# Optimization experiments

Hardware: AMD Instinct MI355X
Metric: run time of the kernel (lower is better)

Reference implementation:

```python
import math
import jax
import jax.numpy as jnp
from jax import lax
import numpy as np

LARGE_NUMBER = 1e10
NEG = -1e30  # finite stand-in for -inf (safe for logaddexp grads)
K = 64
TRAIN_ENSEMBLE = 2


def _init_esp(M, k, dtype):
    # log elementary symmetric polys of the empty set: e_0 = 1, e_r>0 = 0
    return jnp.full((M, k + 1), NEG, dtype).at[:, 0].set(0.0)


def _esp_step(carry, th_col):
    # carry: [M, k+1] log e_r; add one item with logit th_col: e_r <- e_r + w*e_{r-1}
    M = carry.shape[0]
    shifted = jnp.concatenate([jnp.full((M, 1), NEG, carry.dtype), carry[:, :-1]], axis=1)
    new = jnp.logaddexp(carry, shifted + th_col[:, None])
    return new, new


def log_ek_sum(theta, k):
    # sum over rows of log e_k(exp(theta_row)); grad wrt theta = exact-k inclusion marginals
    init = _init_esp(theta.shape[0], k, theta.dtype)
    final, _ = lax.scan(lambda c, t: (_esp_step(c, t)[0], None), init, theta.T)
    return final[:, k].sum()


def marginals_exact_k(theta, k):
    return jax.grad(lambda th: log_ek_sum(th, k))(theta)  # [M, N]


def suffix_esp_table(theta, k):
    # T[j] = log elem. symmetric polys of suffix items j..N-1; shape [N+1, M, k+1]
    init = _init_esp(theta.shape[0], k, theta.dtype)
    _, Ts = lax.scan(_esp_step, init, jnp.flip(theta.T, 0))
    return jnp.flip(jnp.concatenate([init[None], Ts], 0), 0)


def sample_exact_k(theta, k, u):
    # sequential conditional sampling of an exact-k subset (conditional Poisson)
    # theta: [M, N], u: [T, M, N] uniforms -> binary samples [T, M, N]
    M, N = theta.shape
    T = u.shape[0]
    Tab = suffix_esp_table(theta, k)  # [N+1, M, k+1]
    ar = jnp.arange(M)

    def step(r, xs):
        th_col, Tc, Tn, u_col = xs  # [M], [M,k+1], [M,k+1], [T,M]
        num = Tn[ar[None, :], jnp.maximum(r - 1, 0)]  # [T, M]
        den = Tc[ar[None, :], r]
        p = jnp.where(r > 0, jnp.exp(th_col[None, :] + num - den), 0.0)
        inc = (u_col < p)
        return r - inc.astype(r.dtype), inc.astype(theta.dtype)

    r0 = jnp.full((T, M), k, jnp.int32)
    _, incs = lax.scan(step, r0, (theta.T, Tab[:-1], Tab[1:], jnp.moveaxis(u, 2, 0)))
    return jnp.moveaxis(incs, 0, 2)  # [T, M, N]


def setup_inputs():
    key = jax.random.key(0)
    k1, k2 = jax.random.split(key)
    scores = jax.random.normal(k1, (64, 4096, 2), jnp.float32)
    u = jax.random.uniform(k2, (TRAIN_ENSEMBLE, 64 * 2, 4096), jnp.float32)
    return {"scores": scores, "u": u}


def reference(scores, u):
    B, Nmax, E = scores.shape
    times_sampled = TRAIN_ENSEMBLE
    local_k = min(K, Nmax)
    flat = scores.transpose(0, 2, 1).reshape(B * E, Nmax)
    N = 2 ** math.ceil(math.log2(Nmax))
    flat = jnp.pad(flat, ((0, 0), (0, N - Nmax)), constant_values=-LARGE_NUMBER)
    marg = marginals_exact_k(flat, local_k)           # [M, N]
    samples = sample_exact_k(flat, local_k, u)        # [T, M, N]
    # straight-through estimator
    samples = lax.stop_gradient(samples - marg[None]) + marg[None]
    samples = samples[..., :Nmax]
    marg = marg[:, :Nmax]
    new_mask = samples.reshape(times_sampled, B, E, Nmax).transpose(0, 1, 3, 2)
    new_marginals = marg.reshape(B, E, Nmax).transpose(0, 2, 1)
    return new_mask, new_marginals
```

## Files before the change

### kernel.cpp

```cpp
#include <hip/hip_runtime.h>
#include <hip/hip_bf16.h>

#define NROWS 128
#define NCOLS 4096
#define KVAL  64
#define NEGV  (-1e30f)
#define LOG2E 1.4426950408889634f
#define LN2   0.6931471805599453f

__device__ float g_suf[(size_t)NROWS * (NCOLS + 1) * 64];
__device__ float g_pre[(size_t)NROWS * (NCOLS + 1) * 64];
__device__ unsigned long long g_mask[(size_t)2 * NROWS * NCOLS];
__device__ unsigned char g_map  [(size_t)2 * NROWS * 64 * 64];
__device__ unsigned char g_entry[(size_t)2 * NROWS * 64];

__device__ __forceinline__ float shr1z(float x) {
    int r = __builtin_amdgcn_update_dpp(0, __float_as_int(x), 0x138, 0xF, 0xF, true);
    return __int_as_float(r);
}
__device__ __forceinline__ float readlane_f(float v, int lane) {
    return __int_as_float(__builtin_amdgcn_readlane(__float_as_int(v), lane));
}
__device__ __forceinline__ float lae_fast(float a, float b) {
    float mx = fmaxf(a, b);
    float d  = fabsf(a - b);
    float e  = __builtin_amdgcn_exp2f(d * -LOG2E);
    return fmaf(__builtin_amdgcn_logf(1.0f + e), LN2, mx);
}

__device__ __forceinline__ float dpp_sum64(float x) {
#define SSTEP(ctrl, rmask) { int t_ = __builtin_amdgcn_update_dpp(0, \
        __float_as_int(x), ctrl, rmask, 0xF, false); x = x + __int_as_float(t_); }
    SSTEP(0x111, 0xF) SSTEP(0x112, 0xF) SSTEP(0x114, 0xF) SSTEP(0x118, 0xF)
    SSTEP(0x142, 0xA) SSTEP(0x143, 0xC)
#undef SSTEP
    return readlane_f(x, 63);
}

__global__ __launch_bounds__(64) void dp_kernel(const float* __restrict__ scores) {
    int blk = blockIdx.x;
    int l = threadIdx.x;
    bool suf = (blk < NROWS);
    int m = suf ? blk : (blk - NROWS);
    float* __restrict__ tab = (suf ? g_suf : g_pre) + (size_t)m * (NCOLS + 1) * 64;
    const float* __restrict__ srow = scores + (size_t)(m >> 1) * (NCOLS * 2) + (m & 1);

    tab[(size_t)(suf ? NCOLS : 0) * 64 + l] = NEGV;
    float s = NEGV;
    if (suf) {
        float tile = srow[(size_t)(NCOLS - 64 + l) * 2];
        for (int t0 = NCOLS - 64; t0 >= 0; t0 -= 64) {
            float nxt = (t0 >= 64) ? srow[(size_t)(t0 - 64 + l) * 2] : 0.0f;
            #pragma unroll
            for (int ss = 63; ss >= 0; --ss) {
                float tht = readlane_f(tile, ss);
                float b = shr1z(s) + tht;
                s = lae_fast(s, b);
                tab[(size_t)(t0 + ss) * 64 + l] = s;
            }
            tile = nxt;
        }
    } else {
        float tile = srow[(size_t)l * 2];
        for (int t0 = 0; t0 < NCOLS; t0 += 64) {
            float nxt = (t0 + 64 < NCOLS) ? srow[(size_t)(t0 + 64 + l) * 2] : 0.0f;
            #pragma unroll
            for (int ss = 0; ss < 64; ++ss) {
                float tht = readlane_f(tile, ss);
                float b = shr1z(s) + tht;
                s = lae_fast(s, b);
                tab[(size_t)(t0 + ss + 1) * 64 + l] = s;
            }
            tile = nxt;
        }
    }
}

__global__ __launch_bounds__(256) void maskA_kernel(const float* __restrict__ scores,
                                                    const float* __restrict__ u) {
    int l = threadIdx.x & 63;
    int wid = threadIdx.x >> 6;
    int unit = blockIdx.x * 4 + wid;
    int m  = unit >> 6;
    int b  = unit & 63;
    int t0 = b << 6;
    const float* __restrict__ S = g_suf + (size_t)m * (NCOLS + 1) * 64;
    const float* __restrict__ srow = scores + (size_t)(m >> 1) * (NCOLS * 2) + (m & 1);
    const float* __restrict__ u0 = u + (size_t)m * NCOLS;
    const float* __restrict__ u1 = u + (size_t)(NROWS + m) * NCOLS;

    float R[65];
    #pragma unroll
    for (int j = 0; j <= 64; ++j) R[j] = S[(size_t)(t0 + j) * 64 + l];

    unsigned long long acc0 = 0, acc1 = 0;
    #pragma unroll
    for (int ss = 0; ss < 64; ++ss) {
        int t = t0 + ss;
        float num = shr1z(R[ss + 1]);
        float den = R[ss];
        float tht = srow[(size_t)t * 2];
        float p = __builtin_amdgcn_exp2f(((num + tht) - den) * LOG2E);
        unsigned long long b0 = __ballot(u0[t] < p);
        unsigned long long b1 = __ballot(u1[t] < p);
        acc0 = (l == ss) ? b0 : acc0;
        acc1 = (l == ss) ? b1 : acc1;
    }
    g_mask[(size_t)m * NCOLS + t0 + l] = acc0;
    g_mask[(size_t)(NROWS + m) * NCOLS + t0 + l] = acc1;

    unsigned int a0lo = (unsigned int)acc0, a0hi = (unsigned int)(acc0 >> 32);
    unsigned int a1lo = (unsigned int)acc1, a1hi = (unsigned int)(acc1 >> 32);
    int r0 = l + 1, r1 = l + 1;
    #pragma unroll
    for (int ss = 0; ss < 64; ++ss) {
        unsigned int m0lo = (unsigned int)__builtin_amdgcn_readlane((int)a0lo, ss);
        unsigned int m0hi = (unsigned int)__builtin_amdgcn_readlane((int)a0hi, ss);
        unsigned int m1lo = (unsigned int)__builtin_amdgcn_readlane((int)a1lo, ss);
        unsigned int m1hi = (unsigned int)__builtin_amdgcn_readlane((int)a1hi, ss);
        unsigned long long msk0 = ((unsigned long long)m0hi << 32) | m0lo;
        unsigned long long msk1 = ((unsigned long long)m1hi << 32) | m1lo;
        int inc0 = (r0 > 0) ? (int)((msk0 >> (r0 - 1)) & 1ULL) : 0;
        int inc1 = (r1 > 0) ? (int)((msk1 >> (r1 - 1)) & 1ULL) : 0;
        r0 -= inc0;
        r1 -= inc1;
    }
    g_map[((size_t)m * 64 + b) * 64 + l] = (unsigned char)r0;
    g_map[((size_t)(NROWS + m) * 64 + b) * 64 + l] = (unsigned char)r1;
}

__global__ __launch_bounds__(256) void scanB_kernel() {
    int c = threadIdx.x;
    int r = KVAL;
    for (int b = 0; b < 64; ++b) {
        g_entry[(size_t)c * 64 + b] = (unsigned char)r;
        int nxt = g_map[((size_t)c * 64 + b) * 64 + (r - 1)];
        r = (r > 0) ? nxt : 0;
    }
}

__global__ __launch_bounds__(256) void scanC_kernel(float* __restrict__ out) {
    int l = threadIdx.x & 63;
    int wid = threadIdx.x >> 6;
    int unit = blockIdx.x * 4 + wid;
    int c = unit >> 6;
    int b = unit & 63;
    int tens = c >> 7;
    int m = c & (NROWS - 1);
    const unsigned long long* __restrict__ gm = g_mask + (size_t)c * NCOLS + b * 64;
    float* __restrict__ orow = out + (((size_t)tens * 64 + (m >> 1)) * NCOLS) * 2 + (m & 1);

    unsigned long long tile = gm[l];
    unsigned int tlo = (unsigned int)tile;
    unsigned int thi = (unsigned int)(tile >> 32);
    int r = g_entry[(size_t)c * 64 + b];
    int myinc = 0;
    #pragma unroll
    for (int ss = 0; ss < 64; ++ss) {
        unsigned int slo = (unsigned int)__builtin_amdgcn_readlane((int)tlo, ss);
        unsigned int shi = (unsigned int)__builtin_amdgcn_readlane((int)thi, ss);
        unsigned long long msk = ((unsigned long long)shi << 32) | slo;
        int inc = (r > 0) ? (int)((msk >> (r - 1)) & 1ULL) : 0;
        myinc = (ss == l) ? inc : myinc;
        r -= inc;
    }
    orow[(size_t)(b * 64 + l) * 2] = (float)myinc;
}

__global__ __launch_bounds__(256) void marg_kernel(const float* __restrict__ scores,
                                                   float* __restrict__ out) {
    int l = threadIdx.x & 63;
    int wid = threadIdx.x >> 6;
    int unit = blockIdx.x * 4 + wid;
    int m  = unit >> 6;
    int t0 = (unit & 63) << 6;
    size_t rowbase = (size_t)m * (NCOLS + 1) * 64;
    const float* __restrict__ P = g_pre + rowbase;
    const float* __restrict__ S = g_suf + rowbase;
    const float* __restrict__ srow = scores + (size_t)(m >> 1) * (NCOLS * 2) + (m & 1);
    float den_full = P[(size_t)NCOLS * 64 + 63];

    float mres = 0.0f;
    #pragma unroll 4
    for (int j = 0; j < 64; ++j) {
        int i = t0 + j;
        float vP = (l == 0)  ? 0.0f : P[(size_t)i * 64 + (l - 1)];
        float vS = (l == 63) ? 0.0f : S[(size_t)(i + 1) * 64 + (62 - l)];
        float c  = srow[(size_t)i * 2] - den_full;
        float term = __builtin_amdgcn_exp2f((vP + vS + c) * LOG2E);
        float mg = dpp_sum64(term);
        mres = (l == j) ? mg : mres;
    }
    size_t obase = (size_t)2 * 64 * NCOLS * 2;
    out[obase + ((size_t)(m >> 1) * NCOLS + (t0 + l)) * 2 + (m & 1)] = mres;
}

extern "C" void kernel_launch(void* const* d_in, const int* in_sizes, int n_in,
                              void* d_out, int out_size, void* d_ws, size_t ws_size,
                              hipStream_t stream) {
    const float* scores = (const float*)d_in[0];
    const float* u      = (const float*)d_in[1];
    float* out = (float*)d_out;

    dp_kernel<<<2 * NROWS, 64, 0, stream>>>(scores);
    maskA_kernel<<<2048, 256, 0, stream>>>(scores, u);
    scanB_kernel<<<1, 256, 0, stream>>>();
    scanC_kernel<<<4096, 256, 0, stream>>>(out);
    marg_kernel<<<2048, 256, 0, stream>>>(scores, out);
}
```

Measured before the change: 273.4 us.

## Fuse marginal computation into maskA kernel reusing suffix-table registers

New measurement: 258.6 us. 1.06x faster.

```diff
diff --git a/kernel.cpp b/kernel.cpp
--- a/kernel.cpp
+++ b/kernel.cpp
@@ -77,14 +77,17 @@
 }
 
 __global__ __launch_bounds__(256) void maskA_kernel(const float* __restrict__ scores,
-                                                    const float* __restrict__ u) {
+                                                    const float* __restrict__ u,
+                                                    float* __restrict__ out) {
     int l = threadIdx.x & 63;
     int wid = threadIdx.x >> 6;
     int unit = blockIdx.x * 4 + wid;
     int m  = unit >> 6;
     int b  = unit & 63;
     int t0 = b << 6;
-    const float* __restrict__ S = g_suf + (size_t)m * (NCOLS + 1) * 64;
+    size_t rowbase = (size_t)m * (NCOLS + 1) * 64;
+    const float* __restrict__ S = g_suf + rowbase;
+    const float* __restrict__ P = g_pre + rowbase;
     const float* __restrict__ srow = scores + (size_t)(m >> 1) * (NCOLS * 2) + (m & 1);
     const float* __restrict__ u0 = u + (size_t)m * NCOLS;
     const float* __restrict__ u1 = u + (size_t)(NROWS + m) * NCOLS;
@@ -93,7 +96,16 @@
     #pragma unroll
     for (int j = 0; j <= 64; ++j) R[j] = S[(size_t)(t0 + j) * 64 + l];
 
+    float den_full = P[(size_t)NCOLS * 64 + 63];
+
+    int pidx = (l < 63) ? (62 - l) : 62;
+    float ring[16];
+    #pragma unroll
+    for (int j = 0; j < 16; ++j)
+        ring[j] = P[(size_t)(t0 + j) * 64 + pidx];
+
     unsigned long long acc0 = 0, acc1 = 0;
+    float mres = 0.0f;
     #pragma unroll
     for (int ss = 0; ss < 64; ++ss) {
         int t = t0 + ss;
@@ -105,9 +117,18 @@
         unsigned long long b1 = __ballot(u1[t] < p);
         acc0 = (l == ss) ? b0 : acc0;
         acc1 = (l == ss) ? b1 : acc1;
+        float vP = (l == 63) ? 0.0f : ring[ss & 15];
+        int inext = t + 16;
+        if (inext > NCOLS) inext = NCOLS;
+        ring[ss & 15] = P[(size_t)inext * 64 + pidx];
+        float term = __builtin_amdgcn_exp2f((vP + num + (tht - den_full)) * LOG2E);
+        float mg = dpp_sum64(term);
+        mres = (l == ss) ? mg : mres;
     }
     g_mask[(size_t)m * NCOLS + t0 + l] = acc0;
     g_mask[(size_t)(NROWS + m) * NCOLS + t0 + l] = acc1;
+    size_t obase = (size_t)2 * 64 * NCOLS * 2;
+    out[obase + ((size_t)(m >> 1) * NCOLS + (t0 + l)) * 2 + (m & 1)] = mres;
 
     unsigned int a0lo = (unsigned int)acc0, a0hi = (unsigned int)(acc0 >> 32);
     unsigned int a1lo = (unsigned int)acc1, a1hi = (unsigned int)(acc1 >> 32);
@@ -167,34 +188,6 @@
     orow[(size_t)(b * 64 + l) * 2] = (float)myinc;
 }
 
-__global__ __launch_bounds__(256) void marg_kernel(const float* __restrict__ scores,
-                                                   float* __restrict__ out) {
-    int l = threadIdx.x & 63;
-    int wid = threadIdx.x >> 6;
-    int unit = blockIdx.x * 4 + wid;
-    int m  = unit >> 6;
-    int t0 = (unit & 63) << 6;
-    size_t rowbase = (size_t)m * (NCOLS + 1) * 64;
-    const float* __restrict__ P = g_pre + rowbase;
-    const float* __restrict__ S = g_suf + rowbase;
-    const float* __restrict__ srow = scores + (size_t)(m >> 1) * (NCOLS * 2) + (m & 1);
-    float den_full = P[(size_t)NCOLS * 64 + 63];
-
-    float mres = 0.0f;
-    #pragma unroll 4
-    for (int j = 0; j < 64; ++j) {
-        int i = t0 + j;
-        float vP = (l == 0)  ? 0.0f : P[(size_t)i * 64 + (l - 1)];
-        float vS = (l == 63) ? 0.0f : S[(size_t)(i + 1) * 64 + (62 - l)];
-        float c  = srow[(size_t)i * 2] - den_full;
-        float term = __builtin_amdgcn_exp2f((vP + vS + c) * LOG2E);
-        float mg = dpp_sum64(term);
-        mres = (l == j) ? mg : mres;
-    }
-    size_t obase = (size_t)2 * 64 * NCOLS * 2;
-    out[obase + ((size_t)(m >> 1) * NCOLS + (t0 + l)) * 2 + (m & 1)] = mres;
-}
-
 extern "C" void kernel_launch(void* const* d_in, const int* in_sizes, int n_in,
                               void* d_out, int out_size, void* d_ws, size_t ws_size,
                               hipStream_t stream) {
@@ -203,8 +196,7 @@
     float* out = (float*)d_out;
 
     dp_kernel<<<2 * NROWS, 64, 0, stream>>>(scores);
-    maskA_kernel<<<2048, 256, 0, stream>>>(scores, u);
+    maskA_kernel<<<2048, 256, 0, stream>>>(scores, u, out);
     scanB_kernel<<<1, 256, 0, stream>>>();
     scanC_kernel<<<4096, 256, 0, stream>>>(out);
-    marg_kernel<<<2048, 256, 0, stream>>>(scores, out);
-}
+}
```
